# Performance work log

Measured on AMD Instinct MI355X. Metric: run time of the kernel, lower is better.

Reference implementation:

```python
import jax, jax.numpy as jnp
import numpy as np

B, T, SD = 16, 512, 64          # batch, action seq len, sample_dim
EMB, HD = 1024, 64              # emb_dim, head_dim
NH = EMB // HD                  # 16 heads
DEPTH, NREG, LAT, FF = 8, 16, 256, 4 * EMB
S = T + NREG                    # total sequence length (actions + registers)


def setup_inputs() -> dict:
    key = jax.random.key(0)
    ks = jax.random.split(key, 16)
    def n(k, shape, scale=0.02):
        return jax.random.normal(k, shape, jnp.float32) * scale
    return {
        "sample": jax.random.normal(ks[0], (B, T, SD), jnp.float32),
        "W_emb": n(ks[1], (SD, EMB)), "b_emb": jnp.zeros((EMB,), jnp.float32),
        "pos": n(ks[2], (T, EMB)),
        "registers": n(ks[3], (NREG, EMB), 1.0),
        "ln1_s": jnp.ones((DEPTH, EMB), jnp.float32), "ln1_b": jnp.zeros((DEPTH, EMB), jnp.float32),
        "W_qkv": n(ks[4], (DEPTH, EMB, 3 * EMB)), "b_qkv": jnp.zeros((DEPTH, 3 * EMB), jnp.float32),
        "W_o": n(ks[5], (DEPTH, EMB, EMB)), "b_o": jnp.zeros((DEPTH, EMB), jnp.float32),
        "ln2_s": jnp.ones((DEPTH, EMB), jnp.float32), "ln2_b": jnp.zeros((DEPTH, EMB), jnp.float32),
        "W_fc1": n(ks[6], (DEPTH, EMB, FF)), "b_fc1": jnp.zeros((DEPTH, FF), jnp.float32),
        "W_fc2": n(ks[7], (DEPTH, FF, EMB)), "b_fc2": jnp.zeros((DEPTH, EMB), jnp.float32),
        "lnf_s": jnp.ones((EMB,), jnp.float32), "lnf_b": jnp.zeros((EMB,), jnp.float32),
        "W_head": n(ks[8], (EMB, LAT)), "b_head": jnp.zeros((LAT,), jnp.float32),
    }


def _ln(x, s, b):
    m = jnp.mean(x, -1, keepdims=True)
    v = jnp.var(x, -1, keepdims=True)
    return (x - m) * jax.lax.rsqrt(v + 1e-5) * s + b


def _causal_last_mask():
    # True = attended to. Actions attend to all actions but NOT registers;
    # registers attend to all actions and causally (incl. self) to registers.
    allowed = jnp.ones((S, S), jnp.bool_)
    allowed = allowed.at[:T, T:].set(False)
    allowed = allowed.at[T:, T:].set(jnp.tril(jnp.ones((NREG, NREG), jnp.bool_)))
    return allowed


def reference(sample, W_emb, b_emb, pos, registers, ln1_s, ln1_b, W_qkv, b_qkv,
              W_o, b_o, ln2_s, ln2_b, W_fc1, b_fc1, W_fc2, b_fc2,
              lnf_s, lnf_b, W_head, b_head):
    # embed + positional add
    x = sample @ W_emb + b_emb + pos[None, :, :]          # [B,T,E]
    # concat registers
    x = jnp.concatenate([x, jnp.broadcast_to(registers, (B, NREG, EMB))], axis=1)  # [B,S,E]
    mask = _causal_last_mask()                             # [S,S]
    scale = 1.0 / jnp.sqrt(jnp.asarray(HD, x.dtype))
    for i in range(DEPTH):
        # pre-LN multi-head attention with structured block mask
        h = _ln(x, ln1_s[i], ln1_b[i])
        qkv = h @ W_qkv[i] + b_qkv[i]
        q, k, v = jnp.split(qkv, 3, axis=-1)
        q = q.reshape(B, S, NH, HD)
        k = k.reshape(B, S, NH, HD)
        v = v.reshape(B, S, NH, HD)
        att = jnp.einsum('bqhd,bkhd->bhqk', q, k) * scale
        att = jnp.where(mask[None, None], att, jnp.finfo(att.dtype).min)
        att = jax.nn.softmax(att, axis=-1)
        o = jnp.einsum('bhqk,bkhd->bqhd', att, v).reshape(B, S, EMB)
        x = x + o @ W_o[i] + b_o[i]
        # pre-LN MLP
        h2 = _ln(x, ln2_s[i], ln2_b[i])
        x = x + jax.nn.gelu(h2 @ W_fc1[i] + b_fc1[i]) @ W_fc2[i] + b_fc2[i]
    x = _ln(x, lnf_s, lnf_b)
    # head applied to register positions only
    return x[:, T:] @ W_head + b_head                      # [B,NREG,LAT]
```

## Files before the change

kernel.cpp:

```cpp
#include <hip/hip_runtime.h>
#include <hip/hip_bf16.h>


typedef unsigned short u16;
typedef __attribute__((ext_vector_type(4))) float f32x4;
typedef __attribute__((ext_vector_type(8))) __bf16 bf16x8;

#define DEV static __device__ __forceinline__

constexpr int Bb = 16, Tt = 512, E = 1024, HD = 64, NHd = 16;
constexpr int DEPTH = 8, NREG = 16, LAT = 256, FF = 4096;
constexpr int S = Tt + NREG;
constexpr int SPAD = 576;
constexpr int MR = Bb * S;
constexpr int ME = Bb * Tt;

DEV u16 f2bf(float f) {
  unsigned u = __builtin_bit_cast(unsigned, f);
  u += 0x7fffu + ((u >> 16) & 1u);
  return (u16)(u >> 16);
}
DEV float bf2f(u16 h) { return __builtin_bit_cast(float, (unsigned)h << 16); }

DEV void gll16(const u16* g, u16* l) {
  __builtin_amdgcn_global_load_lds((const __attribute__((address_space(1))) void*)g,
                                   (__attribute__((address_space(3))) void*)l, 16, 0, 0);
}

enum { M_EMBED, M_QKV, M_OPROJ, M_FC1, M_FC2, M_HEAD };

struct GA {
  const u16* A; const u16* Bt;
  int K, lda, ldb, Nrows, ldc;
  const float* bias; const float* pos;
  float* fout; u16* bout;
  u16 *qp, *kp, *vtp;
};

template<int MODE, int BN>
__global__ __launch_bounds__(256)
void gemm_bt(GA g) {
  constexpr int NI = BN / 32;
  __shared__ __align__(16) u16 As[3][128 * 32];
  __shared__ __align__(16) u16 Bs[3][BN * 32];
  const int tid = threadIdx.x;
  const u16* A  = g.A;
  const u16* Bt = g.Bt;

  int tM, tN;
  {
    const int nwg = gridDim.x * gridDim.y;
    int flat = blockIdx.y * gridDim.x + blockIdx.x;
    const int q = nwg >> 3, r = nwg & 7;
    const int xcd = flat & 7, loc = flat >> 3;
    flat = (xcd < r ? xcd * (q + 1) : r * (q + 1) + (xcd - r) * q) + loc;
    tM = flat / gridDim.x; tN = flat % gridDim.x;
  }

  const int lane = tid & 63, wid = tid >> 6;
  const int wr = wid >> 1, wc = wid & 1;
  const int fr = lane & 15, fg = lane >> 4;

  const int arow = tM * 128 + (tid >> 2);
  int br0 = tN * BN + (tid >> 2);
  if (br0 > g.Nrows - 1) br0 = g.Nrows - 1;
  int br1 = tN * BN + 64 + (tid >> 2);
  if (br1 > g.Nrows - 1) br1 = g.Nrows - 1;
  const int kseg = ((tid & 3) ^ ((tid >> 3) & 3)) * 8;
  const int woff = (tid & 192) * 8;

  const u16* ag0 = A  + (long)arow        * g.lda + kseg;
  const u16* ag1 = A  + (long)(arow + 64) * g.lda + kseg;
  const u16* bg0 = Bt + (long)br0         * g.ldb + kseg;
  const u16* bg1 = Bt + (long)br1         * g.ldb + kseg;

  f32x4 acc[4][NI];
#pragma unroll
  for (int i = 0; i < 4; ++i)
#pragma unroll
    for (int j = 0; j < NI; ++j) acc[i][j] = f32x4{0.f, 0.f, 0.f, 0.f};

#define STAGE(KT, BUF) do {                                   \
    const int _k0 = (KT) << 5;                                \
    gll16(ag0 + _k0, &As[BUF][woff]);                         \
    gll16(ag1 + _k0, &As[BUF][woff + 2048]);                  \
    gll16(bg0 + _k0, &Bs[BUF][woff]);                         \
    if (BN == 128) gll16(bg1 + _k0, &Bs[BUF][woff + 2048]);   \
  } while (0)

  const int nk = g.K >> 5;
  STAGE(0, 0);
  if (nk > 1) STAGE(1, 1);

  const int rsw = (fg ^ ((fr >> 1) & 3)) * 8;
  constexpr int LPS = (BN == 128) ? 4 : 3;

  for (int kt = 0; kt < nk; ++kt) {
    const int cur = kt % 3;
    if (kt < nk - 1) {
      asm volatile("s_waitcnt vmcnt(%0)" :: "i"(LPS) : "memory");
    } else {
      asm volatile("s_waitcnt vmcnt(0)" ::: "memory");
    }
    __builtin_amdgcn_sched_barrier(0);
    __builtin_amdgcn_s_barrier();
    __builtin_amdgcn_sched_barrier(0);
    if (kt + 2 < nk) STAGE(kt + 2, (kt + 2) % 3);

    bf16x8 af[4], bfr[NI];
#pragma unroll
    for (int mi = 0; mi < 4; ++mi)
      af[mi] = *(const bf16x8*)&As[cur][(wr * 64 + mi * 16 + fr) * 32 + rsw];
#pragma unroll
    for (int ni = 0; ni < NI; ++ni)
      bfr[ni] = *(const bf16x8*)&Bs[cur][(wc * (BN / 2) + ni * 16 + fr) * 32 + rsw];
    __builtin_amdgcn_s_setprio(1);
#pragma unroll
    for (int mi = 0; mi < 4; ++mi)
#pragma unroll
      for (int ni = 0; ni < NI; ++ni)
        acc[mi][ni] = __builtin_amdgcn_mfma_f32_16x16x32_bf16(af[mi], bfr[ni], acc[mi][ni], 0, 0, 0);
    __builtin_amdgcn_s_setprio(0);
  }
#undef STAGE

#pragma unroll
  for (int mi = 0; mi < 4; ++mi)
#pragma unroll
    for (int ni = 0; ni < NI; ++ni)
#pragma unroll
      for (int j = 0; j < 4; ++j) {
        const int row = tM * 128 + wr * 64 + mi * 16 + fg * 4 + j;
        const int col = tN * BN + wc * (BN / 2) + ni * 16 + fr;
        float v = acc[mi][ni][j];
        if (MODE == M_EMBED) {
          const int b = row >> 9, t = row & 511;
          v += g.bias[col] + g.pos[(long)t * E + col];
          g.fout[((long)(b * S + t)) * E + col] = v;
        } else if (MODE == M_QKV) {
          const int b = row / S, s = row - b * S;
          v += g.bias[col];
          const int part = col >> 10, c = col & 1023;
          const int hh = c >> 6, d = c & 63;
          const u16 bf = f2bf(v);
          if (part == 0)      g.qp [((long)((b * NHd + hh) * SPAD + s)) * HD + d] = bf;
          else if (part == 1) g.kp [((long)((b * NHd + hh) * SPAD + s)) * HD + d] = bf;
          else                g.vtp[((long)((b * NHd + hh) * HD   + d)) * SPAD + s] = bf;
        } else if (MODE == M_OPROJ || MODE == M_FC2) {
          const long idx = (long)row * g.ldc + col;
          g.fout[idx] += v + g.bias[col];
        } else if (MODE == M_FC1) {
          v += g.bias[col];
          const float z = 0.7978845608028654f * (v + 0.044715f * v * v * v);
          const float e = __expf(2.f * z);
          const float th = 1.f - 2.f / (e + 1.f);
          g.bout[(long)row * g.ldc + col] = f2bf(0.5f * v * (1.f + th));
        } else if (MODE == M_HEAD) {
          g.fout[(long)row * g.ldc + col] = v + g.bias[col];
        }
      }
}

__global__ __launch_bounds__(256)
void flash_k(const u16* __restrict__ q, const u16* __restrict__ k,
             const u16* __restrict__ vt, u16* __restrict__ o) {
  __shared__ __align__(16) u16 Ks[2][64 * 64];
  __shared__ __align__(16) u16 Vs[2][64 * 64];
  __shared__ __align__(16) u16 Ps[4 * 32 * 64];
  const int tid = threadIdx.x;
  const int lane = tid & 63, w = tid >> 6;
  const int fr = lane & 15, fg = lane >> 4;

  int flat = blockIdx.y * 5 + blockIdx.x;
  flat = (flat & 7) * 160 + (flat >> 3);
  const int bh = flat / 5, qt = flat % 5;
  const int q0 = qt * 128;

  bf16x8 qf[2][2];
#pragma unroll
  for (int ms = 0; ms < 2; ++ms) {
    int qr = q0 + w * 32 + ms * 16 + fr;
    if (qr > SPAD - 1) qr = SPAD - 1;
    const u16* qrow = q + ((long)bh * SPAD + qr) * HD;
    qf[ms][0] = *(const bf16x8*)(qrow + fg * 8);
    qf[ms][1] = *(const bf16x8*)(qrow + 32 + fg * 8);
  }

  const int srow = lane >> 3;
  const int sseg = (((lane & 7) ^ (srow & 7)) * 8);
  const u16* kg = k  + ((long)bh * SPAD + w * 16 + srow) * HD + sseg;
  const u16* vg = vt + ((long)(bh * HD + w * 16 + srow)) * SPAD + sseg;

#define STAGE_F(KT, BUF) do {                                       \
    gll16(kg + (KT) * 64 * HD,          &Ks[BUF][w * 16 * HD]);     \
    gll16(kg + (KT) * 64 * HD + 8 * HD, &Ks[BUF][w * 16 * HD + 8 * HD]); \
    gll16(vg + (KT) * 64,               &Vs[BUF][w * 16 * HD]);     \
    gll16(vg + (KT) * 64 + 8 * SPAD,    &Vs[BUF][w * 16 * HD + 8 * HD]); \
  } while (0)

  const int frm = fr & 7;

  float m[2][4], lsum[2][4]; f32x4 oa[2][4];
#pragma unroll
  for (int ms = 0; ms < 2; ++ms)
#pragma unroll
    for (int j = 0; j < 4; ++j) { m[ms][j] = -1e30f; lsum[ms][j] = 0.f; }
#pragma unroll
  for (int ms = 0; ms < 2; ++ms)
#pragma unroll
    for (int n = 0; n < 4; ++n) oa[ms][n] = f32x4{0.f, 0.f, 0.f, 0.f};

  const int nt = (qt < 4) ? 8 : 9;
  STAGE_F(0, 0);
  for (int kt = 0; kt < nt; ++kt) {
    const int cur = kt & 1;
    asm volatile("s_waitcnt vmcnt(0)" ::: "memory");
    __builtin_amdgcn_sched_barrier(0);
    __builtin_amdgcn_s_barrier();
    __builtin_amdgcn_sched_barrier(0);
    if (kt + 1 < nt) STAGE_F(kt + 1, cur ^ 1);

    f32x4 sfr[2][4];
#pragma unroll
    for (int n = 0; n < 4; ++n) {
      const bf16x8 kf0 = *(const bf16x8*)&Ks[cur][(n * 16 + fr) * HD + ((fg ^ frm) * 8)];
      const bf16x8 kf1 = *(const bf16x8*)&Ks[cur][(n * 16 + fr) * HD + (((fg + 4) ^ frm) * 8)];
#pragma unroll
      for (int ms = 0; ms < 2; ++ms) {
        sfr[ms][n] = __builtin_amdgcn_mfma_f32_16x16x32_bf16(qf[ms][0], kf0, f32x4{0.f,0.f,0.f,0.f}, 0, 0, 0);
        sfr[ms][n] = __builtin_amdgcn_mfma_f32_16x16x32_bf16(qf[ms][1], kf1, sfr[ms][n], 0, 0, 0);
      }
    }
    float p[2][4][4];
#pragma unroll
    for (int ms = 0; ms < 2; ++ms)
#pragma unroll
      for (int j = 0; j < 4; ++j) {
        const int qg = q0 + w * 32 + ms * 16 + fg * 4 + j;
        const int vlim = qg < Tt ? Tt : qg + 1;
#pragma unroll
        for (int n = 0; n < 4; ++n) {
          const int col = kt * 64 + n * 16 + fr;
          p[ms][n][j] = (col < vlim) ? sfr[ms][n][j] * 0.125f : -1e30f;
        }
      }
#pragma unroll
    for (int ms = 0; ms < 2; ++ms)
#pragma unroll
      for (int j = 0; j < 4; ++j) {
        float pm = fmaxf(fmaxf(p[ms][0][j], p[ms][1][j]), fmaxf(p[ms][2][j], p[ms][3][j]));
#pragma unroll
        for (int msk = 1; msk <= 8; msk <<= 1) pm = fmaxf(pm, __shfl_xor(pm, msk));
        const float mn = fmaxf(m[ms][j], pm);
        const float corr = __expf(m[ms][j] - mn);
        m[ms][j] = mn;
        float rs = 0.f;
#pragma unroll
        for (int n = 0; n < 4; ++n) { const float e = __expf(p[ms][n][j] - mn); p[ms][n][j] = e; rs += e; }
#pragma unroll
        for (int msk = 1; msk <= 8; msk <<= 1) rs += __shfl_xor(rs, msk);
        lsum[ms][j] = lsum[ms][j] * corr + rs;
#pragma unroll
        for (int n = 0; n < 4; ++n) oa[ms][n][j] *= corr;
      }
#pragma unroll
    for (int ms = 0; ms < 2; ++ms)
#pragma unroll
      for (int j = 0; j < 4; ++j) {
        const int r = ms * 16 + fg * 4 + j;
#pragma unroll
        for (int n = 0; n < 4; ++n) {
          const int gr = 2 * n + (fr >> 3);
          Ps[w * 2048 + r * 64 + ((gr ^ (r & 7)) * 8) + frm] = f2bf(p[ms][n][j]);
        }
      }
    asm volatile("s_waitcnt lgkmcnt(0)" ::: "memory");
    __builtin_amdgcn_sched_barrier(0);
    bf16x8 pf[2][2];
#pragma unroll
    for (int ms = 0; ms < 2; ++ms) {
      pf[ms][0] = *(const bf16x8*)&Ps[w * 2048 + (ms * 16 + fr) * 64 + ((fg ^ frm) * 8)];
      pf[ms][1] = *(const bf16x8*)&Ps[w * 2048 + (ms * 16 + fr) * 64 + (((fg + 4) ^ frm) * 8)];
    }
#pragma unroll
    for (int n = 0; n < 4; ++n) {
      const bf16x8 vf0 = *(const bf16x8*)&Vs[cur][(n * 16 + fr) * HD + ((fg ^ frm) * 8)];
      const bf16x8 vf1 = *(const bf16x8*)&Vs[cur][(n * 16 + fr) * HD + (((fg + 4) ^ frm) * 8)];
#pragma unroll
      for (int ms = 0; ms < 2; ++ms) {
        oa[ms][n] = __builtin_amdgcn_mfma_f32_16x16x32_bf16(pf[ms][0], vf0, oa[ms][n], 0, 0, 0);
        oa[ms][n] = __builtin_amdgcn_mfma_f32_16x16x32_bf16(pf[ms][1], vf1, oa[ms][n], 0, 0, 0);
      }
    }
  }
#undef STAGE_F

  const int b = bh >> 4, hh = bh & 15;
#pragma unroll
  for (int ms = 0; ms < 2; ++ms)
#pragma unroll
    for (int j = 0; j < 4; ++j) {
      const int qg = q0 + w * 32 + ms * 16 + fg * 4 + j;
      if (qg < S) {
        const float inv = 1.f / lsum[ms][j];
#pragma unroll
        for (int n = 0; n < 4; ++n)
          o[((long)(b * S + qg)) * E + hh * HD + n * 16 + fr] = f2bf(oa[ms][n][j] * inv);
      }
    }
}

__global__ __launch_bounds__(256)
void ln_k(const float* __restrict__ x, const float* __restrict__ sc,
          const float* __restrict__ bi, u16* __restrict__ out, int gather) {
  const int r = blockIdx.x;
  const int srow = gather ? ((r >> 4) * S + Tt + (r & 15)) : r;
  const float4 v = ((const float4*)(x + (long)srow * E))[threadIdx.x];
  float s = v.x + v.y + v.z + v.w;
  float q = v.x * v.x + v.y * v.y + v.z * v.z + v.w * v.w;
#pragma unroll
  for (int o = 32; o; o >>= 1) { s += __shfl_down(s, o); q += __shfl_down(q, o); }
  __shared__ float ps[8];
  if ((threadIdx.x & 63) == 0) { ps[threadIdx.x >> 6] = s; ps[4 + (threadIdx.x >> 6)] = q; }
  __syncthreads();
  s = ps[0] + ps[1] + ps[2] + ps[3];
  q = ps[4] + ps[5] + ps[6] + ps[7];
  const float mean = s * (1.f / E);
  const float rs = rsqrtf(q * (1.f / E) - mean * mean + 1e-5f);
  const int c = threadIdx.x * 4;
  ushort4 o4;
  o4.x = f2bf((v.x - mean) * rs * sc[c + 0] + bi[c + 0]);
  o4.y = f2bf((v.y - mean) * rs * sc[c + 1] + bi[c + 1]);
  o4.z = f2bf((v.z - mean) * rs * sc[c + 2] + bi[c + 2]);
  o4.w = f2bf((v.w - mean) * rs * sc[c + 3] + bi[c + 3]);
  ((ushort4*)(out + (long)r * E))[threadIdx.x] = o4;
}

__global__ __launch_bounds__(256)
void wtrans(const float* __restrict__ src, u16* __restrict__ dst, int R, int C) {
  __shared__ float t[32][33];
  const int c0 = blockIdx.x * 32, r0 = blockIdx.y * 32;
  const int tx = threadIdx.x & 31, ty = threadIdx.x >> 5;
#pragma unroll
  for (int i = 0; i < 32; i += 8) t[ty + i][tx] = src[(long)(r0 + ty + i) * C + c0 + tx];
  __syncthreads();
#pragma unroll
  for (int i = 0; i < 32; i += 8) dst[(long)(c0 + ty + i) * R + r0 + tx] = f2bf(t[tx][ty + i]);
}

struct WT4 {
  const float* s[4]; u16* d[4];
  int R[4], C[4], tx[4], st[4];
};
__global__ __launch_bounds__(256)
void wtrans4(WT4 a) {
  const int bid = blockIdx.x;
  const int wsel = (bid >= a.st[1]) + (bid >= a.st[2]) + (bid >= a.st[3]);
  const int t = bid - a.st[wsel];
  const int c0 = (t % a.tx[wsel]) * 32, r0 = (t / a.tx[wsel]) * 32;
  const float* src = a.s[wsel]; u16* dst = a.d[wsel];
  const int R = a.R[wsel], C = a.C[wsel];
  __shared__ float tt[32][33];
  const int tx = threadIdx.x & 31, ty = threadIdx.x >> 5;
#pragma unroll
  for (int i = 0; i < 32; i += 8) tt[ty + i][tx] = src[(long)(r0 + ty + i) * C + c0 + tx];
  __syncthreads();
#pragma unroll
  for (int i = 0; i < 32; i += 8) dst[(long)(c0 + ty + i) * R + r0 + tx] = f2bf(tt[tx][ty + i]);
}

__global__ void cvt_bf(const float* __restrict__ in, u16* __restrict__ out, long n) {
  const long i = ((long)blockIdx.x * blockDim.x + threadIdx.x) * 4;
  if (i >= n) return;
  const float4 v = *(const float4*)(in + i);
  ushort4 o; o.x = f2bf(v.x); o.y = f2bf(v.y); o.z = f2bf(v.z); o.w = f2bf(v.w);
  *(ushort4*)(out + i) = o;
}

__global__ void zero_k(float4* p, long n) {
  long i = (long)blockIdx.x * blockDim.x + threadIdx.x;
  const long st = (long)gridDim.x * blockDim.x;
  const float4 z = make_float4(0.f, 0.f, 0.f, 0.f);
  for (; i < n; i += st) p[i] = z;
}

__global__ void reg_copy(const float* __restrict__ regs, float* __restrict__ x) {
  const int b = blockIdx.x >> 4, r = blockIdx.x & 15;
  const float4* sp = (const float4*)(regs + (long)r * E);
  float4* dp = (float4*)(x + ((long)(b * S + Tt + r)) * E);
  dp[threadIdx.x] = sp[threadIdx.x];
}

constexpr long OFF_WQKV = 0L;
constexpr long OFF_WO   = OFF_WQKV + 3072L * 1024 * 2;
constexpr long OFF_WFC1 = OFF_WO   + 1024L * 1024 * 2;
constexpr long OFF_WFC2 = OFF_WFC1 + 4096L * 1024 * 2;
constexpr long OFF_WEMB = OFF_WFC2 + 1024L * 4096 * 2;
constexpr long OFF_WHEAD= OFF_WEMB + 1024L * 64 * 2;
constexpr long OFF_SMP  = OFF_WHEAD+ 256L * 1024 * 2;
constexpr long OFF_X    = OFF_SMP  + (long)ME * 64 * 2;
constexpr long OFF_H    = OFF_X    + (long)MR * E * 4;
constexpr long OFF_Q    = OFF_H    + (long)MR * E * 2;
constexpr long OFF_K    = OFF_Q    + 256L * SPAD * HD * 2;
constexpr long OFF_VT   = OFF_K    + 256L * SPAD * HD * 2;
constexpr long OFF_O    = OFF_VT   + 256L * SPAD * HD * 2;
constexpr long OFF_HF   = OFF_O    + (long)MR * FF * 2;
constexpr long WS_NEED  = OFF_HF   + 256L * 1024 * 2;

extern "C" void kernel_launch(void* const* d_in, const int* in_sizes, int n_in,
                              void* d_out, int out_size, void* d_ws, size_t ws_size,
                              hipStream_t stream) {
  if (ws_size < (size_t)WS_NEED) return;

  const float* sample = (const float*)d_in[0];
  const float* W_emb  = (const float*)d_in[1];
  const float* b_emb  = (const float*)d_in[2];
  const float* pos    = (const float*)d_in[3];
  const float* regs   = (const float*)d_in[4];
  const float* ln1_s  = (const float*)d_in[5];
  const float* ln1_b  = (const float*)d_in[6];
  const float* W_qkv  = (const float*)d_in[7];
  const float* b_qkv  = (const float*)d_in[8];
  const float* W_o    = (const float*)d_in[9];
  const float* b_o    = (const float*)d_in[10];
  const float* ln2_s  = (const float*)d_in[11];
  const float* ln2_b  = (const float*)d_in[12];
  const float* W_fc1  = (const float*)d_in[13];
  const float* b_fc1  = (const float*)d_in[14];
  const float* W_fc2  = (const float*)d_in[15];
  const float* b_fc2  = (const float*)d_in[16];
  const float* lnf_s  = (const float*)d_in[17];
  const float* lnf_b  = (const float*)d_in[18];
  const float* W_head = (const float*)d_in[19];
  const float* b_head = (const float*)d_in[20];

  char* w = (char*)d_ws;
  u16* wqkvT = (u16*)(w + OFF_WQKV);
  u16* woT   = (u16*)(w + OFF_WO);
  u16* wfc1T = (u16*)(w + OFF_WFC1);
  u16* wfc2T = (u16*)(w + OFF_WFC2);
  u16* wembT = (u16*)(w + OFF_WEMB);
  u16* wheadT= (u16*)(w + OFF_WHEAD);
  u16* smp   = (u16*)(w + OFF_SMP);
  float* x   = (float*)(w + OFF_X);
  u16* h     = (u16*)(w + OFF_H);
  u16* qp    = (u16*)(w + OFF_Q);
  u16* kp    = (u16*)(w + OFF_K);
  u16* vtp   = (u16*)(w + OFF_VT);
  u16* o     = (u16*)(w + OFF_O);
  u16* a1    = (u16*)(w + OFF_O);
  u16* hf    = (u16*)(w + OFF_HF);

  wtrans<<<dim3(32, 2, 1), 256, 0, stream>>>(W_emb,  wembT, 64, 1024);
  wtrans<<<dim3(8, 32, 1), 256, 0, stream>>>(W_head, wheadT, 1024, 256);
  cvt_bf<<<dim3(512), 256, 0, stream>>>(sample, smp, (long)ME * 64);
  zero_k<<<dim3(2048), 256, 0, stream>>>((float4*)qp, (3L * 256 * SPAD * HD * 2) / 16);

  {
    GA g{}; g.A = smp; g.Bt = wembT; g.K = 64; g.lda = 64; g.ldb = 64;
    g.Nrows = E; g.bias = b_emb; g.pos = pos; g.fout = x;
    gemm_bt<M_EMBED, 64><<<dim3(16, 64, 1), 256, 0, stream>>>(g);
  }
  reg_copy<<<dim3(256), 256, 0, stream>>>(regs, x);

  for (int L = 0; L < DEPTH; ++L) {
    {
      WT4 a;
      a.s[0] = W_qkv + (long)L * 1024 * 3072; a.d[0] = wqkvT; a.R[0] = 1024; a.C[0] = 3072; a.tx[0] = 96;  a.st[0] = 0;
      a.s[1] = W_o   + (long)L * 1024 * 1024; a.d[1] = woT;   a.R[1] = 1024; a.C[1] = 1024; a.tx[1] = 32;  a.st[1] = 3072;
      a.s[2] = W_fc1 + (long)L * 1024 * 4096; a.d[2] = wfc1T; a.R[2] = 1024; a.C[2] = 4096; a.tx[2] = 128; a.st[2] = 4096;
      a.s[3] = W_fc2 + (long)L * 4096 * 1024; a.d[3] = wfc2T; a.R[3] = 4096; a.C[3] = 1024; a.tx[3] = 32;  a.st[3] = 8192;
      wtrans4<<<dim3(12288), 256, 0, stream>>>(a);
    }

    ln_k<<<dim3(MR), 256, 0, stream>>>(x, ln1_s + L * E, ln1_b + L * E, h, 0);
    {
      GA g{}; g.A = h; g.Bt = wqkvT;
      g.K = 1024; g.lda = 1024; g.ldb = 1024; g.Nrows = 3072;
      g.bias = b_qkv + L * 3072; g.qp = qp; g.kp = kp; g.vtp = vtp;
      gemm_bt<M_QKV, 128><<<dim3(24, 66, 1), 256, 0, stream>>>(g);
    }
    flash_k<<<dim3(5, 256, 1), 256, 0, stream>>>(qp, kp, vtp, o);
    {
      GA g{}; g.A = o; g.Bt = woT;
      g.K = 1024; g.lda = 1024; g.ldb = 1024; g.Nrows = 1024; g.ldc = 1024;
      g.bias = b_o + L * E; g.fout = x;
      gemm_bt<M_OPROJ, 128><<<dim3(8, 66, 1), 256, 0, stream>>>(g);
    }
    ln_k<<<dim3(MR), 256, 0, stream>>>(x, ln2_s + L * E, ln2_b + L * E, h, 0);
    {
      GA g{}; g.A = h; g.Bt = wfc1T;
      g.K = 1024; g.lda = 1024; g.ldb = 1024; g.Nrows = 4096; g.ldc = 4096;
      g.bias = b_fc1 + L * FF; g.bout = a1;
      gemm_bt<M_FC1, 128><<<dim3(32, 66, 1), 256, 0, stream>>>(g);
    }
    {
      GA g{}; g.A = a1; g.Bt = wfc2T;
      g.K = 4096; g.lda = 4096; g.ldb = 4096; g.Nrows = 1024; g.ldc = 1024;
      g.bias = b_fc2 + L * E; g.fout = x;
      gemm_bt<M_FC2, 128><<<dim3(8, 66, 1), 256, 0, stream>>>(g);
    }
  }

  ln_k<<<dim3(256), 256, 0, stream>>>(x, lnf_s, lnf_b, hf, 1);
  {
    GA g{}; g.A = hf; g.Bt = wheadT; g.K = 1024; g.lda = 1024; g.ldb = 1024;
    g.Nrows = LAT; g.ldc = LAT; g.bias = b_head; g.fout = (float*)d_out;
    gemm_bt<M_HEAD, 64><<<dim3(4, 2, 1), 256, 0, stream>>>(g);
  }
}
```

Before: 3.882 ms.

## Split-K the FC2 GEMM and fuse the partial reduction with the next layer's LayerNorm

FC2 is split into two K-halves across blockIdx.z, doubling the workgroup count. Each half writes bf16 partial sums into the otherwise idle K and V^T scratch buffers. A new red_ln kernel adds both partials plus bias into the fp32 residual and, in the same pass, computes the next layer's LN1, so the separate LN1 launch runs only for layer 0. The aim is better CU fill for the narrow N=1024 GEMM and one fewer full-activation pass per layer. The cost is bf16 rounding of the partial sums, and the scratch writes overwrite the padding rows in the K buffer that were zeroed once at startup.

```diff
diff --git a/kernel.cpp b/kernel.cpp
--- a/kernel.cpp
+++ b/kernel.cpp
@@ -31,7 +31,7 @@
 
 struct GA {
   const u16* A; const u16* Bt;
-  int K, lda, ldb, Nrows, ldc;
+  int K, Kc, lda, ldb, Nrows, ldc;
   const float* bias; const float* pos;
   float* fout; u16* bout;
   u16 *qp, *kp, *vtp;
@@ -44,8 +44,8 @@
   __shared__ __align__(16) u16 As[3][128 * 32];
   __shared__ __align__(16) u16 Bs[3][BN * 32];
   const int tid = threadIdx.x;
-  const u16* A  = g.A;
-  const u16* Bt = g.Bt;
+  const u16* A  = g.A  + (long)blockIdx.z * g.Kc;
+  const u16* Bt = g.Bt + (long)blockIdx.z * g.Kc;
 
   int tM, tN;
   {
@@ -88,7 +88,7 @@
     if (BN == 128) gll16(bg1 + _k0, &Bs[BUF][woff + 2048]);   \
   } while (0)
 
-  const int nk = g.K >> 5;
+  const int nk = g.Kc >> 5;
   STAGE(0, 0);
   if (nk > 1) STAGE(1, 1);
 
@@ -146,9 +146,12 @@
           if (part == 0)      g.qp [((long)((b * NHd + hh) * SPAD + s)) * HD + d] = bf;
           else if (part == 1) g.kp [((long)((b * NHd + hh) * SPAD + s)) * HD + d] = bf;
           else                g.vtp[((long)((b * NHd + hh) * HD   + d)) * SPAD + s] = bf;
-        } else if (MODE == M_OPROJ || MODE == M_FC2) {
+        } else if (MODE == M_OPROJ) {
           const long idx = (long)row * g.ldc + col;
           g.fout[idx] += v + g.bias[col];
+        } else if (MODE == M_FC2) {
+          u16* dst = blockIdx.z ? g.kp : g.qp;
+          dst[(long)row * g.ldc + col] = f2bf(v);
         } else if (MODE == M_FC1) {
           v += g.bias[col];
           const float z = 0.7978845608028654f * (v + 0.044715f * v * v * v);
@@ -159,6 +162,45 @@
           g.fout[(long)row * g.ldc + col] = v + g.bias[col];
         }
       }
+}
+
+template<int DOLN>
+__global__ __launch_bounds__(256)
+void red_ln(float* __restrict__ x, const u16* __restrict__ p0,
+            const u16* __restrict__ p1, const float* __restrict__ bias,
+            const float* __restrict__ sc, const float* __restrict__ bi,
+            u16* __restrict__ out) {
+  const int r = blockIdx.x;
+  const int c4 = threadIdx.x;
+  float4 v = ((const float4*)(x + (long)r * E))[c4];
+  const ushort4 a = ((const ushort4*)(p0 + (long)r * E))[c4];
+  const ushort4 b = ((const ushort4*)(p1 + (long)r * E))[c4];
+  const float4 bb = ((const float4*)bias)[c4];
+  v.x += bb.x + bf2f(a.x) + bf2f(b.x);
+  v.y += bb.y + bf2f(a.y) + bf2f(b.y);
+  v.z += bb.z + bf2f(a.z) + bf2f(b.z);
+  v.w += bb.w + bf2f(a.w) + bf2f(b.w);
+  ((float4*)(x + (long)r * E))[c4] = v;
+  if (DOLN) {
+    float s = v.x + v.y + v.z + v.w;
+    float q = v.x * v.x + v.y * v.y + v.z * v.z + v.w * v.w;
+#pragma unroll
+    for (int o = 32; o; o >>= 1) { s += __shfl_down(s, o); q += __shfl_down(q, o); }
+    __shared__ float ps[8];
+    if ((threadIdx.x & 63) == 0) { ps[threadIdx.x >> 6] = s; ps[4 + (threadIdx.x >> 6)] = q; }
+    __syncthreads();
+    s = ps[0] + ps[1] + ps[2] + ps[3];
+    q = ps[4] + ps[5] + ps[6] + ps[7];
+    const float mean = s * (1.f / E);
+    const float rs = rsqrtf(q * (1.f / E) - mean * mean + 1e-5f);
+    const int c = threadIdx.x * 4;
+    ushort4 o4;
+    o4.x = f2bf((v.x - mean) * rs * sc[c + 0] + bi[c + 0]);
+    o4.y = f2bf((v.y - mean) * rs * sc[c + 1] + bi[c + 1]);
+    o4.z = f2bf((v.z - mean) * rs * sc[c + 2] + bi[c + 2]);
+    o4.w = f2bf((v.w - mean) * rs * sc[c + 3] + bi[c + 3]);
+    ((ushort4*)(out + (long)r * E))[threadIdx.x] = o4;
+  }
 }
 
 __global__ __launch_bounds__(256)
@@ -457,7 +499,7 @@
   zero_k<<<dim3(2048), 256, 0, stream>>>((float4*)qp, (3L * 256 * SPAD * HD * 2) / 16);
 
   {
-    GA g{}; g.A = smp; g.Bt = wembT; g.K = 64; g.lda = 64; g.ldb = 64;
+    GA g{}; g.A = smp; g.Bt = wembT; g.K = 64; g.Kc = 64; g.lda = 64; g.ldb = 64;
     g.Nrows = E; g.bias = b_emb; g.pos = pos; g.fout = x;
     gemm_bt<M_EMBED, 64><<<dim3(16, 64, 1), 256, 0, stream>>>(g);
   }
@@ -473,38 +515,45 @@
       wtrans4<<<dim3(12288), 256, 0, stream>>>(a);
     }
 
-    ln_k<<<dim3(MR), 256, 0, stream>>>(x, ln1_s + L * E, ln1_b + L * E, h, 0);
+    if (L == 0)
+      ln_k<<<dim3(MR), 256, 0, stream>>>(x, ln1_s, ln1_b, h, 0);
     {
       GA g{}; g.A = h; g.Bt = wqkvT;
-      g.K = 1024; g.lda = 1024; g.ldb = 1024; g.Nrows = 3072;
+      g.K = 1024; g.Kc = 1024; g.lda = 1024; g.ldb = 1024; g.Nrows = 3072;
       g.bias = b_qkv + L * 3072; g.qp = qp; g.kp = kp; g.vtp = vtp;
       gemm_bt<M_QKV, 128><<<dim3(24, 66, 1), 256, 0, stream>>>(g);
     }
     flash_k<<<dim3(5, 256, 1), 256, 0, stream>>>(qp, kp, vtp, o);
     {
       GA g{}; g.A = o; g.Bt = woT;
-      g.K = 1024; g.lda = 1024; g.ldb = 1024; g.Nrows = 1024; g.ldc = 1024;
+      g.K = 1024; g.Kc = 1024; g.lda = 1024; g.ldb = 1024; g.Nrows = 1024; g.ldc = 1024;
       g.bias = b_o + L * E; g.fout = x;
       gemm_bt<M_OPROJ, 128><<<dim3(8, 66, 1), 256, 0, stream>>>(g);
     }
     ln_k<<<dim3(MR), 256, 0, stream>>>(x, ln2_s + L * E, ln2_b + L * E, h, 0);
     {
       GA g{}; g.A = h; g.Bt = wfc1T;
-      g.K = 1024; g.lda = 1024; g.ldb = 1024; g.Nrows = 4096; g.ldc = 4096;
+      g.K = 1024; g.Kc = 1024; g.lda = 1024; g.ldb = 1024; g.Nrows = 4096; g.ldc = 4096;
       g.bias = b_fc1 + L * FF; g.bout = a1;
       gemm_bt<M_FC1, 128><<<dim3(32, 66, 1), 256, 0, stream>>>(g);
     }
     {
       GA g{}; g.A = a1; g.Bt = wfc2T;
-      g.K = 4096; g.lda = 4096; g.ldb = 4096; g.Nrows = 1024; g.ldc = 1024;
-      g.bias = b_fc2 + L * E; g.fout = x;
-      gemm_bt<M_FC2, 128><<<dim3(8, 66, 1), 256, 0, stream>>>(g);
-    }
+      g.K = 4096; g.Kc = 2048; g.lda = 4096; g.ldb = 4096; g.Nrows = 1024; g.ldc = 1024;
+      g.qp = kp; g.kp = vtp;
+      gemm_bt<M_FC2, 128><<<dim3(8, 66, 2), 256, 0, stream>>>(g);
+    }
+    if (L < DEPTH - 1)
+      red_ln<1><<<dim3(MR), 256, 0, stream>>>(x, kp, vtp, b_fc2 + L * E,
+                                              ln1_s + (L + 1) * E, ln1_b + (L + 1) * E, h);
+    else
+      red_ln<0><<<dim3(MR), 256, 0, stream>>>(x, kp, vtp, b_fc2 + L * E,
+                                              lnf_s, lnf_b, h);
   }
 
   ln_k<<<dim3(256), 256, 0, stream>>>(x, lnf_s, lnf_b, hf, 1);
   {
-    GA g{}; g.A = hf; g.Bt = wheadT; g.K = 1024; g.lda = 1024; g.ldb = 1024;
+    GA g{}; g.A = hf; g.Bt = wheadT; g.K = 1024; g.Kc = 1024; g.lda = 1024; g.ldb = 1024;
     g.Nrows = LAT; g.ldc = LAT; g.bias = b_head; g.fout = (float*)d_out;
     gemm_bt<M_HEAD, 64><<<dim3(4, 2, 1), 256, 0, stream>>>(g);
   }
```

Measured after the change: 3.832 ms. No clear change (-1.3%).
